# Performance work log

Hardware: AMD Instinct MI355X
Metric: run time of the kernel (lower is better)

The kernel has to match this reference:

```python
import jax, jax.numpy as jnp
import numpy as np

DILATIONS = (1, 2, 4, 8, 12, 24)
W1 = 0.3
W2 = 0.01
EPS = 1e-8
# 8 neighbor taps of a 3x3 kernel, center excluded; (row, col) indices in {0,1,2}
OFFSETS = ((0, 0), (0, 1), (0, 2), (1, 0), (1, 2), (2, 0), (2, 1), (2, 2))
# distance weights: sqrt(2) on diagonals (taps 0,2,5,7), 1 on axial taps
_DIAG = np.array([np.sqrt(2), 1, np.sqrt(2), 1, 1, np.sqrt(2), 1, np.sqrt(2)], dtype=np.float32)


def get_pos():
    # [1,1,K,1,1] with K = 8*len(DILATIONS); dilation-major ordering matches torch cat
    pos = np.concatenate([_DIAG * d for d in DILATIONS]).astype(np.float32)
    return jnp.asarray(pos)[None, None, :, None, None]


def dilated_neighbors(x):
    # x: [b,c,h,w] -> [b,c,K,h,w]; replicate-pad then shifted slices emulate the
    # one-hot depthwise dilated conv gather (same dilation-major, tap-minor order).
    b, c, h, w = x.shape
    outs = []
    for d in DILATIONS:
        xp = jnp.pad(x, ((0, 0), (0, 0), (d, d), (d, d)), mode='edge')
        for (i, j) in OFFSETS:
            outs.append(jax.lax.dynamic_slice(xp, (0, 0, i * d, j * d), (b, c, h, w)))
    return jnp.stack(outs, axis=2)


def _std(x, axis):
    # torch.std default: unbiased (ddof=1), keepdim=True here
    n = x.shape[axis]
    m = jnp.mean(x, axis=axis, keepdims=True)
    v = jnp.sum((x - m) ** 2, axis=axis, keepdims=True) / (n - 1)
    return jnp.sqrt(v)


def setup_inputs() -> dict:
    key = jax.random.key(0)
    imgs = jax.random.normal(key, (4, 3, 384, 384), dtype=jnp.float32)
    return {"imgs": imgs}


def reference(imgs):
    b, c, h, w = imgs.shape
    nb = dilated_neighbors(imgs)                 # [b,c,K,h,w]
    pos = get_pos()                              # [1,1,K,1,1]
    d_abs = jnp.abs(nb - imgs[:, :, None])       # [b,c,K,h,w]
    img_std = _std(nb, axis=2)                   # [b,c,1,h,w]
    pos_std = _std(pos, axis=2)                  # [1,1,1,1,1]
    aff = -jnp.mean((d_abs / (img_std + EPS) / W1) ** 2, axis=1, keepdims=True)  # [b,1,K,h,w]
    pos_aff = -((pos / (pos_std + EPS) / W1) ** 2)                               # [1,1,K,1,1]
    out = jax.nn.softmax(aff, axis=2) + W2 * jax.nn.softmax(pos_aff, axis=2)
    return out  # [b,1,K,h,w]
```

## Files before the change

kernel.cpp:

```cpp
#include <hip/hip_runtime.h>
#include <math.h>

#define IMG_H  384
#define IMG_W  384
#define IMG_HW (IMG_H * IMG_W)
#define NB     4
#define NC     3
#define NK     48
#define NH     24

struct PosAdd { float v[NK]; };

__global__ __launch_bounds__(256) void LLA_41412074668179_kernel(
    const float* __restrict__ imgs, float* __restrict__ out, PosAdd pa)
{
    const int tid  = threadIdx.x;
    const int lane = tid & 63;
    const int t    = lane >> 5;
    const int px   = blockIdx.x * 128 + (tid >> 6) * 32 + (lane & 31);
    const int w  = px % IMG_W;
    const int hb = px / IMG_W;
    const int h  = hb % IMG_H;
    const int b  = hb / IMG_H;

    const int dils[3] = { t ? 8 : 1, t ? 12 : 2, t ? 24 : 4 };

    const int r0 = h * IMG_W;
    int rm[3], rp[3], cm[3], cp[3];
#pragma unroll
    for (int di = 0; di < 3; ++di) {
        const int d = dils[di];
        rm[di] = max(h - d, 0) * IMG_W;
        rp[di] = min(h + d, IMG_H - 1) * IMG_W;
        cm[di] = max(w - d, 0);
        cp[di] = min(w + d, IMG_W - 1);
    }

    float acc[NH];
#pragma unroll
    for (int j = 0; j < NH; ++j) acc[j] = 0.0f;

#pragma unroll
    for (int c = 0; c < NC; ++c) {
        const float* __restrict__ pc = imgs + ((size_t)b * NC + c) * IMG_HW;
        const float x = pc[r0 + w];

        float nbv[NH];
#pragma unroll
        for (int di = 0; di < 3; ++di) {
            nbv[di*8+0] = pc[rm[di] + cm[di]];
            nbv[di*8+1] = pc[rm[di] + w];
            nbv[di*8+2] = pc[rm[di] + cp[di]];
            nbv[di*8+3] = pc[r0     + cm[di]];
            nbv[di*8+4] = pc[r0     + cp[di]];
            nbv[di*8+5] = pc[rp[di] + cm[di]];
            nbv[di*8+6] = pc[rp[di] + w];
            nbv[di*8+7] = pc[rp[di] + cp[di]];
        }

        float s0 = 0.0f, s1 = 0.0f, q0 = 0.0f, q1 = 0.0f;
#pragma unroll
        for (int j = 0; j < NH; j += 2) {
            s0 += nbv[j];
            s1 += nbv[j+1];
            q0 = fmaf(nbv[j],   nbv[j],   q0);
            q1 = fmaf(nbv[j+1], nbv[j+1], q1);
        }
        float s  = s0 + s1;
        float ss = q0 + q1;
        s  += __shfl_xor(s, 32);
        ss += __shfl_xor(ss, 32);

        const float mean = s * (1.0f / 48.0f);
        const float var  = fmaxf((ss - s * mean) * (1.0f / 47.0f), 0.0f);
        const float scl  = __builtin_amdgcn_rcpf(
                               fmaf(__builtin_amdgcn_sqrtf(var), 0.3f, 3.0e-9f));
        const float xs = x * scl;

#pragma unroll
        for (int j = 0; j < NH; ++j) {
            const float d = fmaf(nbv[j], scl, -xs);
            acc[j] = fmaf(d, d, acc[j]);
        }
    }

    float m0 = fminf(acc[0], acc[1]), m1 = fminf(acc[2], acc[3]);
    float m2 = fminf(acc[4], acc[5]), m3 = fminf(acc[6], acc[7]);
#pragma unroll
    for (int j = 8; j < NH; j += 8) {
        m0 = fminf(m0, fminf(acc[j+0], acc[j+1]));
        m1 = fminf(m1, fminf(acc[j+2], acc[j+3]));
        m2 = fminf(m2, fminf(acc[j+4], acc[j+5]));
        m3 = fminf(m3, fminf(acc[j+6], acc[j+7]));
    }
    float mn = fminf(fminf(m0, m1), fminf(m2, m3));
    mn = fminf(mn, __shfl_xor(mn, 32));

    const float SC   = (1.0f / 3.0f) * 1.44269504f;
    const float mnSC = mn * SC;
    float e0 = 0.0f, e1 = 0.0f, e2 = 0.0f, e3 = 0.0f;
#pragma unroll
    for (int j = 0; j < NH; j += 4) {
        acc[j+0] = __builtin_amdgcn_exp2f(fmaf(acc[j+0], -SC, mnSC));
        acc[j+1] = __builtin_amdgcn_exp2f(fmaf(acc[j+1], -SC, mnSC));
        acc[j+2] = __builtin_amdgcn_exp2f(fmaf(acc[j+2], -SC, mnSC));
        acc[j+3] = __builtin_amdgcn_exp2f(fmaf(acc[j+3], -SC, mnSC));
        e0 += acc[j+0]; e1 += acc[j+1]; e2 += acc[j+2]; e3 += acc[j+3];
    }
    float se = (e0 + e1) + (e2 + e3);
    se += __shfl_xor(se, 32);
    const float inv = __builtin_amdgcn_rcpf(se);

    float* __restrict__ op = out + ((size_t)(b * NK + t * NH)) * IMG_HW + r0 + w;
#pragma unroll
    for (int j = 0; j < NH; ++j) {
        const float pav = t ? pa.v[NH + j] : pa.v[j];
        __builtin_nontemporal_store(fmaf(acc[j], inv, pav),
                                    op + (size_t)j * IMG_HW);
    }
}

static void compute_pos_add(float* out48)
{
    const int DIL[6] = {1, 2, 4, 8, 12, 24};
    const double SQ2 = 1.4142135623730951;
    const double diag[8] = {SQ2, 1.0, SQ2, 1.0, 1.0, SQ2, 1.0, SQ2};

    double pos[NK];
    for (int di = 0; di < 6; ++di)
        for (int tp = 0; tp < 8; ++tp)
            pos[di * 8 + tp] = (double)((float)(diag[tp] * DIL[di]));

    double s = 0.0;
    for (int k = 0; k < NK; ++k) s += pos[k];
    const double m = s / NK;
    double v = 0.0;
    for (int k = 0; k < NK; ++k) { const double d = pos[k] - m; v += d * d; }
    v /= (NK - 1);
    const double stdv = sqrt(v);

    double aff[NK];
    double mx = -1e300;
    for (int k = 0; k < NK; ++k) {
        const double q = pos[k] / ((stdv + 1e-8) * 0.3);
        aff[k] = -(q * q);
        if (aff[k] > mx) mx = aff[k];
    }
    double se = 0.0;
    for (int k = 0; k < NK; ++k) { aff[k] = exp(aff[k] - mx); se += aff[k]; }
    for (int k = 0; k < NK; ++k) out48[k] = (float)(0.01 * aff[k] / se);
}

extern "C" void kernel_launch(void* const* d_in, const int* in_sizes, int n_in,
                              void* d_out, int out_size, void* d_ws, size_t ws_size,
                              hipStream_t stream)
{
    const float* imgs = (const float*)d_in[0];
    float* out = (float*)d_out;

    PosAdd pa;
    compute_pos_add(pa.v);

    const int blocks = (NB * IMG_H * IMG_W * 2) / 256;
    LLA_41412074668179_kernel<<<blocks, 256, 0, stream>>>(imgs, out, pa);
}
```

Baseline: 32.12 us.

## Process four pixels per thread with vectorized float4 loads and stores

Each thread now handles four adjacent pixels, using 16-byte (unaligned-typed) vector loads for the shifted neighbor gathers, with scalar clamped fallback at image borders, and 128-bit nontemporal stores for the output. Block indices are remapped with an interleaved swizzle across 8 groups, and the grid shrinks by four. The aim is fewer memory instructions and better store width on a write-bound kernel. In exchange, register use roughly quadruples (96 accumulators plus 96 neighbor values), which may cut occupancy or cause spills, and misaligned vector loads for odd dilations may split across cache lines.

```diff
diff --git a/kernel.cpp b/kernel.cpp
--- a/kernel.cpp
+++ b/kernel.cpp
@@ -9,7 +9,44 @@
 #define NK     48
 #define NH     24
 
+typedef float f4  __attribute__((ext_vector_type(4)));
+typedef float f4u __attribute__((ext_vector_type(4), aligned(4)));
+
 struct PosAdd { float v[NK]; };
+
+__device__ __forceinline__ f4 ld4(const float* __restrict__ p) {
+    return (f4)(*(const f4u* __restrict__)p);
+}
+
+__device__ __forceinline__ f4 ldL(const float* __restrict__ rowp, int w0, int d) {
+    if (w0 >= d) return ld4(rowp + (w0 - d));
+    f4 r;
+#pragma unroll
+    for (int i = 0; i < 4; ++i) r[i] = rowp[max(w0 + i - d, 0)];
+    return r;
+}
+
+__device__ __forceinline__ f4 ldR(const float* __restrict__ rowp, int w0, int d) {
+    if (w0 + d <= IMG_W - 4) return ld4(rowp + (w0 + d));
+    f4 r;
+#pragma unroll
+    for (int i = 0; i < 4; ++i) r[i] = rowp[min(w0 + i + d, IMG_W - 1)];
+    return r;
+}
+
+__device__ __forceinline__ f4 min4(f4 a, f4 b) {
+    f4 r;
+#pragma unroll
+    for (int i = 0; i < 4; ++i) r[i] = fminf(a[i], b[i]);
+    return r;
+}
+
+__device__ __forceinline__ f4 exp2_4(f4 v) {
+    f4 r;
+#pragma unroll
+    for (int i = 0; i < 4; ++i) r[i] = __builtin_amdgcn_exp2f(v[i]);
+    return r;
+}
 
 __global__ __launch_bounds__(256) void LLA_41412074668179_kernel(
     const float* __restrict__ imgs, float* __restrict__ out, PosAdd pa)
@@ -17,106 +54,127 @@
     const int tid  = threadIdx.x;
     const int lane = tid & 63;
     const int t    = lane >> 5;
-    const int px   = blockIdx.x * 128 + (tid >> 6) * 32 + (lane & 31);
-    const int w  = px % IMG_W;
-    const int hb = px / IMG_W;
+
+    const int lb = (blockIdx.x & 7) * 144 + (blockIdx.x >> 3);
+
+    const int px0 = lb * 512 + (tid >> 6) * 128 + (lane & 31) * 4;
+    const int w0 = px0 % IMG_W;
+    const int hb = px0 / IMG_W;
     const int h  = hb % IMG_H;
     const int b  = hb / IMG_H;
 
     const int dils[3] = { t ? 8 : 1, t ? 12 : 2, t ? 24 : 4 };
 
     const int r0 = h * IMG_W;
-    int rm[3], rp[3], cm[3], cp[3];
+    int rm[3], rp[3];
 #pragma unroll
     for (int di = 0; di < 3; ++di) {
         const int d = dils[di];
         rm[di] = max(h - d, 0) * IMG_W;
         rp[di] = min(h + d, IMG_H - 1) * IMG_W;
-        cm[di] = max(w - d, 0);
-        cp[di] = min(w + d, IMG_W - 1);
-    }
-
-    float acc[NH];
-#pragma unroll
-    for (int j = 0; j < NH; ++j) acc[j] = 0.0f;
+    }
+
+    f4 acc[NH];
+#pragma unroll
+    for (int j = 0; j < NH; ++j) acc[j] = (f4){0.0f, 0.0f, 0.0f, 0.0f};
 
 #pragma unroll
     for (int c = 0; c < NC; ++c) {
         const float* __restrict__ pc = imgs + ((size_t)b * NC + c) * IMG_HW;
-        const float x = pc[r0 + w];
-
-        float nbv[NH];
+        const f4 x = ld4(pc + r0 + w0);
+
+        f4 nbv[NH];
 #pragma unroll
         for (int di = 0; di < 3; ++di) {
-            nbv[di*8+0] = pc[rm[di] + cm[di]];
-            nbv[di*8+1] = pc[rm[di] + w];
-            nbv[di*8+2] = pc[rm[di] + cp[di]];
-            nbv[di*8+3] = pc[r0     + cm[di]];
-            nbv[di*8+4] = pc[r0     + cp[di]];
-            nbv[di*8+5] = pc[rp[di] + cm[di]];
-            nbv[di*8+6] = pc[rp[di] + w];
-            nbv[di*8+7] = pc[rp[di] + cp[di]];
-        }
-
-        float s0 = 0.0f, s1 = 0.0f, q0 = 0.0f, q1 = 0.0f;
+            const int d = dils[di];
+            const float* __restrict__ pm = pc + rm[di];
+            const float* __restrict__ p0 = pc + r0;
+            const float* __restrict__ pp = pc + rp[di];
+            nbv[di*8+0] = ldL(pm, w0, d);
+            nbv[di*8+1] = ld4(pm + w0);
+            nbv[di*8+2] = ldR(pm, w0, d);
+            nbv[di*8+3] = ldL(p0, w0, d);
+            nbv[di*8+4] = ldR(p0, w0, d);
+            nbv[di*8+5] = ldL(pp, w0, d);
+            nbv[di*8+6] = ld4(pp + w0);
+            nbv[di*8+7] = ldR(pp, w0, d);
+        }
+
+        f4 s0 = (f4){0,0,0,0}, s1 = (f4){0,0,0,0};
+        f4 q0 = (f4){0,0,0,0}, q1 = (f4){0,0,0,0};
 #pragma unroll
         for (int j = 0; j < NH; j += 2) {
             s0 += nbv[j];
             s1 += nbv[j+1];
-            q0 = fmaf(nbv[j],   nbv[j],   q0);
-            q1 = fmaf(nbv[j+1], nbv[j+1], q1);
-        }
-        float s  = s0 + s1;
-        float ss = q0 + q1;
-        s  += __shfl_xor(s, 32);
-        ss += __shfl_xor(ss, 32);
-
-        const float mean = s * (1.0f / 48.0f);
-        const float var  = fmaxf((ss - s * mean) * (1.0f / 47.0f), 0.0f);
-        const float scl  = __builtin_amdgcn_rcpf(
-                               fmaf(__builtin_amdgcn_sqrtf(var), 0.3f, 3.0e-9f));
-        const float xs = x * scl;
+            q0 += nbv[j]   * nbv[j];
+            q1 += nbv[j+1] * nbv[j+1];
+        }
+        f4 s  = s0 + s1;
+        f4 ss = q0 + q1;
+#pragma unroll
+        for (int i = 0; i < 4; ++i) {
+            s[i]  += __shfl_xor(s[i],  32);
+            ss[i] += __shfl_xor(ss[i], 32);
+        }
+
+        f4 scl;
+#pragma unroll
+        for (int i = 0; i < 4; ++i) {
+            const float mean = s[i] * (1.0f / 48.0f);
+            const float var  = fmaxf((ss[i] - s[i] * mean) * (1.0f / 47.0f), 0.0f);
+            scl[i] = __builtin_amdgcn_rcpf(
+                         fmaf(__builtin_amdgcn_sqrtf(var), 0.3f, 3.0e-9f));
+        }
+        const f4 xs = x * scl;
 
 #pragma unroll
         for (int j = 0; j < NH; ++j) {
-            const float d = fmaf(nbv[j], scl, -xs);
-            acc[j] = fmaf(d, d, acc[j]);
-        }
-    }
-
-    float m0 = fminf(acc[0], acc[1]), m1 = fminf(acc[2], acc[3]);
-    float m2 = fminf(acc[4], acc[5]), m3 = fminf(acc[6], acc[7]);
+            const f4 dd = nbv[j] * scl - xs;
+            acc[j] += dd * dd;
+        }
+    }
+
+    f4 m0 = min4(acc[0], acc[1]), m1 = min4(acc[2], acc[3]);
+    f4 m2 = min4(acc[4], acc[5]), m3 = min4(acc[6], acc[7]);
 #pragma unroll
     for (int j = 8; j < NH; j += 8) {
-        m0 = fminf(m0, fminf(acc[j+0], acc[j+1]));
-        m1 = fminf(m1, fminf(acc[j+2], acc[j+3]));
-        m2 = fminf(m2, fminf(acc[j+4], acc[j+5]));
-        m3 = fminf(m3, fminf(acc[j+6], acc[j+7]));
-    }
-    float mn = fminf(fminf(m0, m1), fminf(m2, m3));
-    mn = fminf(mn, __shfl_xor(mn, 32));
+        m0 = min4(m0, min4(acc[j+0], acc[j+1]));
+        m1 = min4(m1, min4(acc[j+2], acc[j+3]));
+        m2 = min4(m2, min4(acc[j+4], acc[j+5]));
+        m3 = min4(m3, min4(acc[j+6], acc[j+7]));
+    }
+    f4 mn = min4(min4(m0, m1), min4(m2, m3));
+#pragma unroll
+    for (int i = 0; i < 4; ++i)
+        mn[i] = fminf(mn[i], __shfl_xor(mn[i], 32));
 
     const float SC   = (1.0f / 3.0f) * 1.44269504f;
-    const float mnSC = mn * SC;
-    float e0 = 0.0f, e1 = 0.0f, e2 = 0.0f, e3 = 0.0f;
+    const f4 mnSC = mn * SC;
+    f4 e0 = (f4){0,0,0,0}, e1 = (f4){0,0,0,0};
+    f4 e2 = (f4){0,0,0,0}, e3 = (f4){0,0,0,0};
 #pragma unroll
     for (int j = 0; j < NH; j += 4) {
-        acc[j+0] = __builtin_amdgcn_exp2f(fmaf(acc[j+0], -SC, mnSC));
-        acc[j+1] = __builtin_amdgcn_exp2f(fmaf(acc[j+1], -SC, mnSC));
-        acc[j+2] = __builtin_amdgcn_exp2f(fmaf(acc[j+2], -SC, mnSC));
-        acc[j+3] = __builtin_amdgcn_exp2f(fmaf(acc[j+3], -SC, mnSC));
+        acc[j+0] = exp2_4(acc[j+0] * -SC + mnSC);
+        acc[j+1] = exp2_4(acc[j+1] * -SC + mnSC);
+        acc[j+2] = exp2_4(acc[j+2] * -SC + mnSC);
+        acc[j+3] = exp2_4(acc[j+3] * -SC + mnSC);
         e0 += acc[j+0]; e1 += acc[j+1]; e2 += acc[j+2]; e3 += acc[j+3];
     }
-    float se = (e0 + e1) + (e2 + e3);
-    se += __shfl_xor(se, 32);
-    const float inv = __builtin_amdgcn_rcpf(se);
-
-    float* __restrict__ op = out + ((size_t)(b * NK + t * NH)) * IMG_HW + r0 + w;
+    f4 se = (e0 + e1) + (e2 + e3);
+#pragma unroll
+    for (int i = 0; i < 4; ++i)
+        se[i] += __shfl_xor(se[i], 32);
+    f4 inv;
+#pragma unroll
+    for (int i = 0; i < 4; ++i)
+        inv[i] = __builtin_amdgcn_rcpf(se[i]);
+
+    float* __restrict__ op = out + ((size_t)(b * NK + t * NH)) * IMG_HW + r0 + w0;
 #pragma unroll
     for (int j = 0; j < NH; ++j) {
         const float pav = t ? pa.v[NH + j] : pa.v[j];
-        __builtin_nontemporal_store(fmaf(acc[j], inv, pav),
-                                    op + (size_t)j * IMG_HW);
+        const f4 v = acc[j] * inv + pav;
+        __builtin_nontemporal_store(v, (f4*)(op + (size_t)j * IMG_HW));
     }
 }
 
@@ -161,6 +219,6 @@
     PosAdd pa;
     compute_pos_add(pa.v);
 
-    const int blocks = (NB * IMG_H * IMG_W * 2) / 256;
+    const int blocks = (NB * IMG_H * IMG_W * 2) / (256 * 4);
     LLA_41412074668179_kernel<<<blocks, 256, 0, stream>>>(imgs, out, pa);
 }
```

New measurement: 50.80 us. 58.1% more time.

## Split each pixel's 48 taps across four lanes instead of two

Applied to the files above, without the earlier changes.

Each pixel is now handled by four lanes, each owning one tap pair per dilation (12 taps), instead of two lanes with 24 taps each. Row, column and position-weight selection is done per slot, and reductions add an extra xor-16 shuffle. The kernel also sets an occupancy hint in launch_bounds and remaps block indices to interleave work across eight groups. This lowers register pressure and raises thread-level parallelism for the gather-heavy loads, at the cost of more shuffles, more threads and output stores that are less contiguous per wavefront.

```diff
diff --git a/kernel.cpp b/kernel.cpp
--- a/kernel.cpp
+++ b/kernel.cpp
@@ -7,68 +7,78 @@
 #define NB     4
 #define NC     3
 #define NK     48
-#define NH     24
+#define ND     6
 
 struct PosAdd { float v[NK]; };
 
-__global__ __launch_bounds__(256) void LLA_41412074668179_kernel(
+
+__global__ __launch_bounds__(256, 8) void LLA_41412074668179_kernel(
     const float* __restrict__ imgs, float* __restrict__ out, PosAdd pa)
 {
     const int tid  = threadIdx.x;
     const int lane = tid & 63;
-    const int t    = lane >> 5;
-    const int px   = blockIdx.x * 128 + (tid >> 6) * 32 + (lane & 31);
+    const int slot = lane >> 4;
+    const bool s0 = slot & 1;
+    const bool s1 = (slot >> 1) & 1;
+
+    const int lb = (blockIdx.x & 7) * 1152 + (blockIdx.x >> 3);
+
+    const int px = lb * 64 + (tid >> 6) * 16 + (lane & 15);
     const int w  = px % IMG_W;
     const int hb = px / IMG_W;
     const int h  = hb % IMG_H;
     const int b  = hb / IMG_H;
+    const int r0 = h * IMG_W;
 
-    const int dils[3] = { t ? 8 : 1, t ? 12 : 2, t ? 24 : 4 };
+    const int DIL[ND] = {1, 2, 4, 8, 12, 24};
 
-    const int r0 = h * IMG_W;
-    int rm[3], rp[3], cm[3], cp[3];
+    int offU[ND], offV[ND];
 #pragma unroll
-    for (int di = 0; di < 3; ++di) {
-        const int d = dils[di];
-        rm[di] = max(h - d, 0) * IMG_W;
-        rp[di] = min(h + d, IMG_H - 1) * IMG_W;
-        cm[di] = max(w - d, 0);
-        cp[di] = min(w + d, IMG_W - 1);
+    for (int di = 0; di < ND; ++di) {
+        const int d  = DIL[di];
+        const int rm = max(h - d, 0) * IMG_W;
+        const int rp = min(h + d, IMG_H - 1) * IMG_W;
+        const int cm = max(w - d, 0);
+        const int cp = min(w + d, IMG_W - 1);
+        const int rowU = s1 ? (s0 ? rp : r0) : rm;
+        const int rowV = s1 ? rp : (s0 ? r0 : rm);
+        const int colU = s1 ? (s0 ? w  : cp) : (s0 ? cp : cm);
+        const int colV = s1 ? (s0 ? cp : cm) : (s0 ? cm : w);
+        offU[di] = rowU + colU;
+        offV[di] = rowV + colV;
     }
+    const int xoff = r0 + w;
 
-    float acc[NH];
+    float accU[ND], accV[ND];
 #pragma unroll
-    for (int j = 0; j < NH; ++j) acc[j] = 0.0f;
+    for (int di = 0; di < ND; ++di) { accU[di] = 0.0f; accV[di] = 0.0f; }
 
 #pragma unroll
     for (int c = 0; c < NC; ++c) {
-        const float* __restrict__ pc = imgs + ((size_t)b * NC + c) * IMG_HW;
-        const float x = pc[r0 + w];
+        const float* __restrict__ pc = imgs + (b * NC + c) * IMG_HW;
 
-        float nbv[NH];
+        const float x = pc[xoff];
+        float u[ND], v[ND];
 #pragma unroll
-        for (int di = 0; di < 3; ++di) {
-            nbv[di*8+0] = pc[rm[di] + cm[di]];
-            nbv[di*8+1] = pc[rm[di] + w];
-            nbv[di*8+2] = pc[rm[di] + cp[di]];
-            nbv[di*8+3] = pc[r0     + cm[di]];
-            nbv[di*8+4] = pc[r0     + cp[di]];
-            nbv[di*8+5] = pc[rp[di] + cm[di]];
-            nbv[di*8+6] = pc[rp[di] + w];
-            nbv[di*8+7] = pc[rp[di] + cp[di]];
+        for (int di = 0; di < ND; ++di) {
+            u[di] = pc[offU[di]];
+            v[di] = pc[offV[di]];
         }
 
-        float s0 = 0.0f, s1 = 0.0f, q0 = 0.0f, q1 = 0.0f;
+        float s  = 0.0f, ss = 0.0f;
+        float s2 = 0.0f, ss2 = 0.0f;
 #pragma unroll
-        for (int j = 0; j < NH; j += 2) {
-            s0 += nbv[j];
-            s1 += nbv[j+1];
-            q0 = fmaf(nbv[j],   nbv[j],   q0);
-            q1 = fmaf(nbv[j+1], nbv[j+1], q1);
+        for (int di = 0; di < ND; di += 2) {
+            s   += u[di]   + v[di];
+            s2  += u[di+1] + v[di+1];
+            ss  = fmaf(u[di],   u[di],   fmaf(v[di],   v[di],   ss));
+            ss2 = fmaf(u[di+1], u[di+1], fmaf(v[di+1], v[di+1], ss2));
         }
-        float s  = s0 + s1;
-        float ss = q0 + q1;
-        s  += __shfl_xor(s, 32);
+        s  += s2;
+        ss += ss2;
+        s  += __shfl_xor(s,  16);
+        s  += __shfl_xor(s,  32);
+        ss += __shfl_xor(ss, 16);
         ss += __shfl_xor(ss, 32);
 
         const float mean = s * (1.0f / 48.0f);
@@ -78,45 +88,48 @@
         const float xs = x * scl;
 
 #pragma unroll
-        for (int j = 0; j < NH; ++j) {
-            const float d = fmaf(nbv[j], scl, -xs);
-            acc[j] = fmaf(d, d, acc[j]);
+        for (int di = 0; di < ND; ++di) {
+            const float du = fmaf(u[di], scl, -xs);
+            const float dv = fmaf(v[di], scl, -xs);
+            accU[di] = fmaf(du, du, accU[di]);
+            accV[di] = fmaf(dv, dv, accV[di]);
         }
     }
 
-    float m0 = fminf(acc[0], acc[1]), m1 = fminf(acc[2], acc[3]);
-    float m2 = fminf(acc[4], acc[5]), m3 = fminf(acc[6], acc[7]);
-#pragma unroll
-    for (int j = 8; j < NH; j += 8) {
-        m0 = fminf(m0, fminf(acc[j+0], acc[j+1]));
-        m1 = fminf(m1, fminf(acc[j+2], acc[j+3]));
-        m2 = fminf(m2, fminf(acc[j+4], acc[j+5]));
-        m3 = fminf(m3, fminf(acc[j+6], acc[j+7]));
-    }
+    float m0 = fminf(accU[0], accV[0]), m1 = fminf(accU[1], accV[1]);
+    float m2 = fminf(accU[2], accV[2]), m3 = fminf(accU[3], accV[3]);
+    m0 = fminf(m0, fminf(accU[4], accV[4]));
+    m1 = fminf(m1, fminf(accU[5], accV[5]));
     float mn = fminf(fminf(m0, m1), fminf(m2, m3));
+    mn = fminf(mn, __shfl_xor(mn, 16));
     mn = fminf(mn, __shfl_xor(mn, 32));
 
     const float SC   = (1.0f / 3.0f) * 1.44269504f;
     const float mnSC = mn * SC;
-    float e0 = 0.0f, e1 = 0.0f, e2 = 0.0f, e3 = 0.0f;
+    float e0 = 0.0f, e1 = 0.0f;
 #pragma unroll
-    for (int j = 0; j < NH; j += 4) {
-        acc[j+0] = __builtin_amdgcn_exp2f(fmaf(acc[j+0], -SC, mnSC));
-        acc[j+1] = __builtin_amdgcn_exp2f(fmaf(acc[j+1], -SC, mnSC));
-        acc[j+2] = __builtin_amdgcn_exp2f(fmaf(acc[j+2], -SC, mnSC));
-        acc[j+3] = __builtin_amdgcn_exp2f(fmaf(acc[j+3], -SC, mnSC));
-        e0 += acc[j+0]; e1 += acc[j+1]; e2 += acc[j+2]; e3 += acc[j+3];
+    for (int di = 0; di < ND; ++di) {
+        accU[di] = __builtin_amdgcn_exp2f(fmaf(accU[di], -SC, mnSC));
+        accV[di] = __builtin_amdgcn_exp2f(fmaf(accV[di], -SC, mnSC));
+        e0 += accU[di];
+        e1 += accV[di];
     }
-    float se = (e0 + e1) + (e2 + e3);
+    float se = e0 + e1;
+    se += __shfl_xor(se, 16);
     se += __shfl_xor(se, 32);
     const float inv = __builtin_amdgcn_rcpf(se);
 
-    float* __restrict__ op = out + ((size_t)(b * NK + t * NH)) * IMG_HW + r0 + w;
+    float* __restrict__ ob = out + (size_t)(b * NK + 2 * slot) * IMG_HW + xoff;
 #pragma unroll
-    for (int j = 0; j < NH; ++j) {
-        const float pav = t ? pa.v[NH + j] : pa.v[j];
-        __builtin_nontemporal_store(fmaf(acc[j], inv, pav),
-                                    op + (size_t)j * IMG_HW);
+    for (int di = 0; di < ND; ++di) {
+        const float paU = s1 ? (s0 ? pa.v[di*8+6] : pa.v[di*8+4])
+                             : (s0 ? pa.v[di*8+2] : pa.v[di*8+0]);
+        const float paV = s1 ? (s0 ? pa.v[di*8+7] : pa.v[di*8+5])
+                             : (s0 ? pa.v[di*8+3] : pa.v[di*8+1]);
+        __builtin_nontemporal_store(fmaf(accU[di], inv, paU),
+                                    ob + (size_t)(di * 8)     * IMG_HW);
+        __builtin_nontemporal_store(fmaf(accV[di], inv, paV),
+                                    ob + (size_t)(di * 8 + 1) * IMG_HW);
     }
 }
 
@@ -161,6 +174,6 @@
     PosAdd pa;
     compute_pos_add(pa.v);
 
-    const int blocks = (NB * IMG_H * IMG_W * 2) / 256;
+    const int blocks = (NB * IMG_H * IMG_W * 4) / 256;
     LLA_41412074668179_kernel<<<blocks, 256, 0, stream>>>(imgs, out, pa);
 }
```

After: 43.39 us. 1.35x slower.

## Stage dilated neighbor rows in LDS and compute all 48 taps per thread

Applied to the files above, without the earlier changes.

Each block now handles half an image row (192 pixels). It cooperatively loads the 13 needed rows per channel, with a 24-column replicate-padded halo, into shared memory using float4 loads, then gathers all neighbor taps from LDS. Each thread now processes all 48 taps for one pixel, which removes the cross-half-wave shuffles the old split required. Blocks are remapped with a swizzle so concurrently running blocks share rows. The cost is higher register pressure from 48 accumulators and an LDS footprint of about 37 KB per block, which may limit occupancy.

```diff
diff --git a/kernel.cpp b/kernel.cpp
--- a/kernel.cpp
+++ b/kernel.cpp
@@ -7,69 +7,102 @@
 #define NB     4
 #define NC     3
 #define NK     48
-#define NH     24
+#define BW     192
+#define SCOLS  240
+#define NROW   13
+#define NSEG   (NC * NROW)
+#define SEGF4  (SCOLS / 4)
+#define TOTF4  (NSEG * SEGF4)
+
+typedef float f4 __attribute__((ext_vector_type(4)));
 
 struct PosAdd { float v[NK]; };
 
-__global__ __launch_bounds__(256) void LLA_41412074668179_kernel(
+__global__ __launch_bounds__(BW, 3) void LLA_41412074668179_kernel(
     const float* __restrict__ imgs, float* __restrict__ out, PosAdd pa)
 {
-    const int tid  = threadIdx.x;
-    const int lane = tid & 63;
-    const int t    = lane >> 5;
-    const int px   = blockIdx.x * 128 + (tid >> 6) * 32 + (lane & 31);
-    const int w  = px % IMG_W;
-    const int hb = px / IMG_W;
-    const int h  = hb % IMG_H;
-    const int b  = hb / IMG_H;
+    const int tid = threadIdx.x;
 
-    const int dils[3] = { t ? 8 : 1, t ? 12 : 2, t ? 24 : 4 };
+    const int lb = (blockIdx.x & 7) * 384 + (blockIdx.x >> 3);
+    const int R  = lb >> 1;
+    const int c0 = (lb & 1) * BW;
+    const int b  = R / IMG_H;
+    const int h  = R - b * IMG_H;
 
-    const int r0 = h * IMG_W;
-    int rm[3], rp[3], cm[3], cp[3];
+    __shared__ __align__(16) float slds[NSEG * SCOLS];
+    __shared__ int gbase[NSEG];
+
+    if (tid < NSEG) {
+        const int c  = (tid >= 26) ? 2 : (tid >= 13 ? 1 : 0);
+        const int ri = tid - c * 13;
+        const int off =
+            ri == 0 ? -24 : ri == 1 ? -12 : ri == 2 ? -8 : ri == 3 ? -4 :
+            ri == 4 ?  -2 : ri == 5 ?  -1 : ri == 6 ?  0 : ri == 7 ?  1 :
+            ri == 8 ?   2 : ri == 9 ?   4 : ri == 10 ? 8 : ri == 11 ? 12 : 24;
+        const int hr = min(max(h + off, 0), IMG_H - 1);
+        gbase[tid] = (b * NC + c) * IMG_HW + hr * IMG_W;
+    }
+    __syncthreads();
+
 #pragma unroll
-    for (int di = 0; di < 3; ++di) {
-        const int d = dils[di];
-        rm[di] = max(h - d, 0) * IMG_W;
-        rp[di] = min(h + d, IMG_H - 1) * IMG_W;
-        cm[di] = max(w - d, 0);
-        cp[di] = min(w + d, IMG_W - 1);
+    for (int k = 0; k < 13; ++k) {
+        const int lin = k * BW + tid;
+        if (lin < TOTF4) {
+            const int s  = lin / SEGF4;
+            const int q  = lin - s * SEGF4;
+            const int g  = c0 - 24 + 4 * q;
+            const int gc = min(max(g, 0), IMG_W - 4);
+            const f4 L0 = *(const f4*)(imgs + gbase[s] + gc);
+            f4 L = (g < 0) ? (f4){L0.x, L0.x, L0.x, L0.x}
+                           : ((g > IMG_W - 4) ? (f4){L0.w, L0.w, L0.w, L0.w} : L0);
+            *(f4*)(slds + s * SCOLS + 4 * q) = L;
+        }
     }
+    __syncthreads();
 
-    float acc[NH];
+    const int wl  = tid;
+    const int ctr = wl + 24;
+    const int DIL[6] = {1, 2, 4, 8, 12, 24};
+
+    float acc[NK];
 #pragma unroll
-    for (int j = 0; j < NH; ++j) acc[j] = 0.0f;
+    for (int j = 0; j < NK; ++j) acc[j] = 0.0f;
 
 #pragma unroll
     for (int c = 0; c < NC; ++c) {
-        const float* __restrict__ pc = imgs + ((size_t)b * NC + c) * IMG_HW;
-        const float x = pc[r0 + w];
+        const float* __restrict__ Lc = slds + c * (NROW * SCOLS);
+        const float x = Lc[6 * SCOLS + ctr];
 
-        float nbv[NH];
+        float nbv[NK];
 #pragma unroll
-        for (int di = 0; di < 3; ++di) {
-            nbv[di*8+0] = pc[rm[di] + cm[di]];
-            nbv[di*8+1] = pc[rm[di] + w];
-            nbv[di*8+2] = pc[rm[di] + cp[di]];
-            nbv[di*8+3] = pc[r0     + cm[di]];
-            nbv[di*8+4] = pc[r0     + cp[di]];
-            nbv[di*8+5] = pc[rp[di] + cm[di]];
-            nbv[di*8+6] = pc[rp[di] + w];
-            nbv[di*8+7] = pc[rp[di] + cp[di]];
+        for (int di = 0; di < 6; ++di) {
+            const int d = DIL[di];
+            const float* __restrict__ rM = Lc + (5 - di) * SCOLS;
+            const float* __restrict__ rC = Lc + 6 * SCOLS;
+            const float* __restrict__ rP = Lc + (7 + di) * SCOLS;
+            nbv[di*8+0] = rM[ctr - d];
+            nbv[di*8+1] = rM[ctr];
+            nbv[di*8+2] = rM[ctr + d];
+            nbv[di*8+3] = rC[ctr - d];
+            nbv[di*8+4] = rC[ctr + d];
+            nbv[di*8+5] = rP[ctr - d];
+            nbv[di*8+6] = rP[ctr];
+            nbv[di*8+7] = rP[ctr + d];
         }
 
-        float s0 = 0.0f, s1 = 0.0f, q0 = 0.0f, q1 = 0.0f;
+        float s0 = 0, s1 = 0, s2 = 0, s3 = 0;
+        float q0 = 0, q1 = 0, q2 = 0, q3 = 0;
 #pragma unroll
-        for (int j = 0; j < NH; j += 2) {
-            s0 += nbv[j];
-            s1 += nbv[j+1];
+        for (int j = 0; j < NK; j += 4) {
+            s0 += nbv[j];   s1 += nbv[j+1];
+            s2 += nbv[j+2]; s3 += nbv[j+3];
             q0 = fmaf(nbv[j],   nbv[j],   q0);
             q1 = fmaf(nbv[j+1], nbv[j+1], q1);
+            q2 = fmaf(nbv[j+2], nbv[j+2], q2);
+            q3 = fmaf(nbv[j+3], nbv[j+3], q3);
         }
-        float s  = s0 + s1;
-        float ss = q0 + q1;
-        s  += __shfl_xor(s, 32);
-        ss += __shfl_xor(ss, 32);
+        const float s  = (s0 + s1) + (s2 + s3);
+        const float ss = (q0 + q1) + (q2 + q3);
 
         const float mean = s * (1.0f / 48.0f);
         const float var  = fmaxf((ss - s * mean) * (1.0f / 47.0f), 0.0f);
@@ -78,44 +111,41 @@
         const float xs = x * scl;
 
 #pragma unroll
-        for (int j = 0; j < NH; ++j) {
-            const float d = fmaf(nbv[j], scl, -xs);
-            acc[j] = fmaf(d, d, acc[j]);
+        for (int j = 0; j < NK; ++j) {
+            const float dd = fmaf(nbv[j], scl, -xs);
+            acc[j] = fmaf(dd, dd, acc[j]);
         }
     }
 
     float m0 = fminf(acc[0], acc[1]), m1 = fminf(acc[2], acc[3]);
     float m2 = fminf(acc[4], acc[5]), m3 = fminf(acc[6], acc[7]);
 #pragma unroll
-    for (int j = 8; j < NH; j += 8) {
+    for (int j = 8; j < NK; j += 8) {
         m0 = fminf(m0, fminf(acc[j+0], acc[j+1]));
         m1 = fminf(m1, fminf(acc[j+2], acc[j+3]));
         m2 = fminf(m2, fminf(acc[j+4], acc[j+5]));
         m3 = fminf(m3, fminf(acc[j+6], acc[j+7]));
     }
-    float mn = fminf(fminf(m0, m1), fminf(m2, m3));
-    mn = fminf(mn, __shfl_xor(mn, 32));
+    const float mn = fminf(fminf(m0, m1), fminf(m2, m3));
 
     const float SC   = (1.0f / 3.0f) * 1.44269504f;
     const float mnSC = mn * SC;
-    float e0 = 0.0f, e1 = 0.0f, e2 = 0.0f, e3 = 0.0f;
+    float e0 = 0, e1 = 0, e2 = 0, e3 = 0;
 #pragma unroll
-    for (int j = 0; j < NH; j += 4) {
+    for (int j = 0; j < NK; j += 4) {
         acc[j+0] = __builtin_amdgcn_exp2f(fmaf(acc[j+0], -SC, mnSC));
         acc[j+1] = __builtin_amdgcn_exp2f(fmaf(acc[j+1], -SC, mnSC));
         acc[j+2] = __builtin_amdgcn_exp2f(fmaf(acc[j+2], -SC, mnSC));
         acc[j+3] = __builtin_amdgcn_exp2f(fmaf(acc[j+3], -SC, mnSC));
         e0 += acc[j+0]; e1 += acc[j+1]; e2 += acc[j+2]; e3 += acc[j+3];
     }
-    float se = (e0 + e1) + (e2 + e3);
-    se += __shfl_xor(se, 32);
+    const float se  = (e0 + e1) + (e2 + e3);
     const float inv = __builtin_amdgcn_rcpf(se);
 
-    float* __restrict__ op = out + ((size_t)(b * NK + t * NH)) * IMG_HW + r0 + w;
+    float* __restrict__ op = out + ((size_t)b * NK) * IMG_HW + h * IMG_W + c0 + wl;
 #pragma unroll
-    for (int j = 0; j < NH; ++j) {
-        const float pav = t ? pa.v[NH + j] : pa.v[j];
-        __builtin_nontemporal_store(fmaf(acc[j], inv, pav),
+    for (int j = 0; j < NK; ++j) {
+        __builtin_nontemporal_store(fmaf(acc[j], inv, pa.v[j]),
                                     op + (size_t)j * IMG_HW);
     }
 }
@@ -161,6 +191,6 @@
     PosAdd pa;
     compute_pos_add(pa.v);
 
-    const int blocks = (NB * IMG_H * IMG_W * 2) / 256;
-    LLA_41412074668179_kernel<<<blocks, 256, 0, stream>>>(imgs, out, pa);
+    const int blocks = NB * IMG_H * 2;
+    LLA_41412074668179_kernel<<<blocks, BW, 0, stream>>>(imgs, out, pa);
 }
```

Measured after the change: 38.69 us. +20.5%, slower.
